# Optimization experiments

Hardware: AMD Instinct MI355X
Metric: run time of the kernel (lower is better)

## Reference

```python
import jax, jax.numpy as jnp
import numpy as np

B, C, H, W = 64, 3, 32, 32
HID, PRE, VMAX = 128, 32, 256
IN_DIM = C * 5 - 1  # 14


def setup_inputs() -> dict:
    key = jax.random.key(0)
    ks = jax.random.split(key, 9)
    s = 0.05
    return {
        "x": jax.random.uniform(ks[0], (B, C, H, W), dtype=jnp.float32),
        "W_pre": jax.random.normal(ks[1], (PRE, IN_DIM), dtype=jnp.float32) * s,
        "b_pre": jnp.zeros((PRE,), dtype=jnp.float32),
        "W_ih": jax.random.normal(ks[2], (3 * HID, PRE), dtype=jnp.float32) * s,
        "b_ih": jnp.zeros((3 * HID,), dtype=jnp.float32),
        "W_hh": jax.random.normal(ks[3], (3 * HID, HID), dtype=jnp.float32) * s,
        "b_hh": jnp.zeros((3 * HID,), dtype=jnp.float32),
        "W_post": jax.random.normal(ks[4], (VMAX, HID), dtype=jnp.float32) * s,
        "b_post": jnp.zeros((VMAX,), dtype=jnp.float32),
    }


def _img2input(x):
    # x: [b, c, h, w] -> [b, (h-2)*(w-2)*c, 5c-1], matching torch _img2input
    b, c, h, w = x.shape
    xp = jnp.transpose(x, (0, 2, 3, 1))  # [b,h,w,c]
    tl = xp[:, :-2, :-2, :]
    tc = xp[:, :-2, 1:-1, :]
    tr = xp[:, :-2, 2:, :]
    lf = xp[:, 1:-1, :-2, :]
    ct = xp[:, 1:-1, 1:-1, :]
    base = jnp.concatenate([tl, tc, tr, lf], axis=-1)  # [b,h-2,w-2,4c]
    base = jnp.broadcast_to(base[..., None, :], base.shape[:3] + (c, 4 * c))
    # tail[ic, ic1] = center[ic1] if ic1 < ic else -1
    mask = jnp.arange(c - 1)[None, :] < jnp.arange(c)[:, None]  # [c, c-1]
    tail = jnp.where(mask, ct[..., None, :c - 1], -1.0)  # [b,h-2,w-2,c,c-1]
    y = jnp.concatenate([base, tail], axis=-1)  # [b,h-2,w-2,c,5c-1]
    return y.reshape(b, (h - 2) * (w - 2) * c, 5 * c - 1)


def reference(x, W_pre, b_pre, W_ih, b_ih, W_hh, b_hh, W_post, b_post):
    b, c, h, w = x.shape
    inp = _img2input(x)                                   # [b, T, 5c-1]
    pre = jax.nn.sigmoid(inp @ W_pre.T + b_pre)           # [b, T, PRE]
    xg = pre @ W_ih.T + b_ih                              # [b, T, 3*HID]
    xg_t = jnp.transpose(xg, (1, 0, 2))                   # [T, b, 3*HID]

    def step(h_prev, xt):
        hg = h_prev @ W_hh.T + b_hh
        xr, xz, xn = jnp.split(xt, 3, axis=-1)
        hr, hz, hn = jnp.split(hg, 3, axis=-1)
        r = jax.nn.sigmoid(xr + hr)
        z = jax.nn.sigmoid(xz + hz)
        n = jnp.tanh(xn + r * hn)
        h_new = (1.0 - z) * n + z * h_prev
        return h_new, h_new

    h0 = jnp.zeros((b, W_hh.shape[1]), dtype=x.dtype)
    _, hs = jax.lax.scan(step, h0, xg_t)                  # [T, b, HID]
    hs = jnp.transpose(hs, (1, 0, 2))                     # [b, T, HID]
    out = hs @ W_post.T + b_post                          # [b, T, VMAX]
    vmax = W_post.shape[0]
    out = out.reshape(b, h - 2, w - 2, c, vmax)
    out = jnp.transpose(out, (0, 3, 1, 2, 4))             # [b, c, h-2, w-2, vmax]
    out = jnp.pad(out, ((0, 0), (0, 0), (1, 1), (1, 1), (0, 0)))
    return out  # [b, c, h, w, vmax]
```

## Files before the change

kernel.cpp:

```cpp
#include <hip/hip_runtime.h>
#include <cstdint>

#define B_    64
#define T_    2700
#define HID_  128
#define PRE_  32
#define VMAX_ 256

typedef _Float16 half2_t __attribute__((ext_vector_type(2)));
typedef _Float16 h8_t    __attribute__((ext_vector_type(8)));
union H8 { h8_t v; half2_t p[4]; };

#if __has_builtin(__builtin_amdgcn_fdot2)
__device__ __forceinline__ float FDOT2(half2_t a, half2_t b, float c) {
    return __builtin_amdgcn_fdot2(a, b, c, false);
}
#else
__device__ __forceinline__ float FDOT2(half2_t a, half2_t b, float c) {
    return c + (float)a[0] * (float)b[0] + (float)a[1] * (float)b[1];
}
#endif

__device__ __forceinline__ half2_t mk2(float a, float b) {
    half2_t r; r[0] = (_Float16)a; r[1] = (_Float16)b; return r;
}

template<int CTRL>
__device__ __forceinline__ float dpp_add(float x) {
    int t = __builtin_amdgcn_update_dpp(0, __float_as_int(x), CTRL, 0xF, 0xF, true);
    return x + __int_as_float(t);
}

__device__ __forceinline__ float fast_sigmoid(float x) {
    float t = __builtin_amdgcn_exp2f(-1.4426950408889634f * x);
    return __builtin_amdgcn_rcpf(1.0f + t);
}
__device__ __forceinline__ float fast_tanh(float x) {
    float t = __builtin_amdgcn_exp2f(2.885390081777927f * x);
    return 1.0f - 2.0f * __builtin_amdgcn_rcpf(t + 1.0f);
}
__device__ __forceinline__ void fma4(float4& a, const float4 w, const float4 h) {
    a.x += w.x * h.x; a.y += w.y * h.y; a.z += w.z * h.z; a.w += w.w * h.w;
}
__device__ __forceinline__ float hsum4(const float4 a) {
    return (a.x + a.y) + (a.z + a.w);
}

__global__ __launch_bounds__(256) void k_pre(const float* __restrict__ x,
                                             const float* __restrict__ W_pre,
                                             const float* __restrict__ b_pre,
                                             float* __restrict__ pre_out) {
    int tid  = blockIdx.x * 256 + threadIdx.x;
    int i    = tid & 31;
    int rest = tid >> 5;
    int c    = rest % 3;
    int r2   = rest / 3;
    int p    = r2 % 900;
    int b    = r2 / 900;
    int r    = p / 30;
    int cc   = p - r * 30;
    const float* xb = x + b * 3072 + r * 32 + cc;
    float f0 = xb[0],    f1  = xb[1024], f2  = xb[2048];
    float f3 = xb[1],    f4  = xb[1025], f5  = xb[2049];
    float f6 = xb[2],    f7  = xb[1026], f8  = xb[2050];
    float f9 = xb[32],   f10 = xb[1056], f11 = xb[2080];
    float ct0 = xb[33],  ct1 = xb[1057];
    float f12 = (c >= 1) ? ct0 : -1.0f;
    float f13 = (c >= 2) ? ct1 : -1.0f;
    const float* w = W_pre + i * 14;
    float d = b_pre[i];
    d += f0*w[0]  + f1*w[1]  + f2*w[2]  + f3*w[3]  + f4*w[4]  + f5*w[5]  + f6*w[6]
       + f7*w[7]  + f8*w[8]  + f9*w[9]  + f10*w[10] + f11*w[11] + f12*w[12] + f13*w[13];
    pre_out[tid] = fast_sigmoid(d);
}

__global__ __launch_bounds__(512, 1) void k_scan(const float* __restrict__ W_ih,
                                                 const float* __restrict__ b_ih,
                                                 const float* __restrict__ W_hh,
                                                 const float* __restrict__ b_hh,
                                                 const float* __restrict__ pre_in,
                                                 float* __restrict__ hs) {
    __shared__ __align__(16) _Float16 sh_h[2][HID_];
    const int tid = threadIdx.x;
    const int u   = tid >> 2;
    const int q   = tid & 3;
    const int b   = blockIdx.x;

    half2_t whr[16], whz[16], whn[16];
    {
        const float4* pr = (const float4*)(W_hh + (size_t)u * HID_ + q * 32);
        const float4* pz = (const float4*)(W_hh + (size_t)(HID_ + u) * HID_ + q * 32);
        const float4* pn = (const float4*)(W_hh + (size_t)(2 * HID_ + u) * HID_ + q * 32);
#pragma unroll
        for (int k = 0; k < 8; ++k) {
            float4 f = pr[k]; whr[2*k] = mk2(f.x, f.y); whr[2*k+1] = mk2(f.z, f.w);
        }
#pragma unroll
        for (int k = 0; k < 8; ++k) {
            float4 f = pz[k]; whz[2*k] = mk2(f.x, f.y); whz[2*k+1] = mk2(f.z, f.w);
        }
#pragma unroll
        for (int k = 0; k < 8; ++k) {
            float4 f = pn[k]; whn[2*k] = mk2(f.x, f.y); whn[2*k+1] = mk2(f.z, f.w);
        }
    }
    half2_t wir[4], wiz[4], win[4];
    {
        const float4* pr = (const float4*)(W_ih + u * PRE_ + q * 8);
        const float4* pz = (const float4*)(W_ih + (HID_ + u) * PRE_ + q * 8);
        const float4* pn = (const float4*)(W_ih + (2 * HID_ + u) * PRE_ + q * 8);
#pragma unroll
        for (int k = 0; k < 2; ++k) {
            float4 f = pr[k]; wir[2*k] = mk2(f.x, f.y); wir[2*k+1] = mk2(f.z, f.w);
            float4 g = pz[k]; wiz[2*k] = mk2(g.x, g.y); wiz[2*k+1] = mk2(g.z, g.w);
            float4 h = pn[k]; win[2*k] = mk2(h.x, h.y); win[2*k+1] = mk2(h.z, h.w);
        }
    }
    const float br  = b_ih[u] + b_hh[u];
    const float bz  = b_ih[HID_ + u] + b_hh[HID_ + u];
    const float bxn = b_ih[2 * HID_ + u];
    const float bhn = b_hh[2 * HID_ + u];

    const float* preb = pre_in + (size_t)b * T_ * PRE_ + q * 8;
    float* hsb = hs + (size_t)b * T_ * HID_;

    if (tid < HID_) { sh_h[0][tid] = (_Float16)0.f; sh_h[1][tid] = (_Float16)0.f; }
    half2_t p[4];
    {
        float4 f0 = ((const float4*)preb)[0];
        float4 f1 = ((const float4*)preb)[1];
        p[0] = mk2(f0.x, f0.y); p[1] = mk2(f0.z, f0.w);
        p[2] = mk2(f1.x, f1.y); p[3] = mk2(f1.z, f1.w);
    }
    float hu = 0.0f;
    __syncthreads();

    for (int t = 0; t < T_; ++t) {
        const int tn = (t + 1 < T_) ? (t + 1) : t;
        const float4* pnx = (const float4*)(preb + (size_t)tn * PRE_);
        float4 nf0 = pnx[0];
        float4 nf1 = pnx[1];

        const h8_t* hblk = (const h8_t*)(&sh_h[t & 1][q * 32]);
        float ar0 = FDOT2(wir[0], p[0], 0.f), ar1 = FDOT2(wir[1], p[1], 0.f);
        ar0 = FDOT2(wir[2], p[2], ar0);       ar1 = FDOT2(wir[3], p[3], ar1);
        float az0 = FDOT2(wiz[0], p[0], 0.f), az1 = FDOT2(wiz[1], p[1], 0.f);
        az0 = FDOT2(wiz[2], p[2], az0);       az1 = FDOT2(wiz[3], p[3], az1);
        float axn0 = FDOT2(win[0], p[0], 0.f), axn1 = FDOT2(win[1], p[1], 0.f);
        axn0 = FDOT2(win[2], p[2], axn0);      axn1 = FDOT2(win[3], p[3], axn1);
        float an0 = 0.f, an1 = 0.f;
#pragma unroll
        for (int k = 0; k < 4; ++k) {
            H8 hb; hb.v = hblk[k];
            ar0 = FDOT2(whr[4*k+0], hb.p[0], ar0);
            ar1 = FDOT2(whr[4*k+1], hb.p[1], ar1);
            ar0 = FDOT2(whr[4*k+2], hb.p[2], ar0);
            ar1 = FDOT2(whr[4*k+3], hb.p[3], ar1);
            az0 = FDOT2(whz[4*k+0], hb.p[0], az0);
            az1 = FDOT2(whz[4*k+1], hb.p[1], az1);
            az0 = FDOT2(whz[4*k+2], hb.p[2], az0);
            az1 = FDOT2(whz[4*k+3], hb.p[3], az1);
            an0 = FDOT2(whn[4*k+0], hb.p[0], an0);
            an1 = FDOT2(whn[4*k+1], hb.p[1], an1);
            an0 = FDOT2(whn[4*k+2], hb.p[2], an0);
            an1 = FDOT2(whn[4*k+3], hb.p[3], an1);
        }
        float sr  = ar0 + ar1;
        float sz  = az0 + az1;
        float sxn = axn0 + axn1;
        float shn = an0 + an1;
        sr  = dpp_add<0x4E>(dpp_add<0xB1>(sr));
        sz  = dpp_add<0x4E>(dpp_add<0xB1>(sz));
        sxn = dpp_add<0x4E>(dpp_add<0xB1>(sxn));
        shn = dpp_add<0x4E>(dpp_add<0xB1>(shn));

        float rg   = fast_sigmoid(sr + br);
        float zg   = fast_sigmoid(sz + bz);
        float ng   = fast_tanh(sxn + bxn + rg * (shn + bhn));
        float hnew = ng + zg * (hu - ng);
        hu = hnew;
        if (q == 0) sh_h[(t + 1) & 1][u] = (_Float16)hnew;
        __syncthreads();
        if (q == 0) hsb[(size_t)t * HID_ + u] = hnew;
        p[0] = mk2(nf0.x, nf0.y); p[1] = mk2(nf0.z, nf0.w);
        p[2] = mk2(nf1.x, nf1.y); p[3] = mk2(nf1.z, nf1.w);
    }
}

__global__ __launch_bounds__(512, 4) void k_post(const float* __restrict__ W_post,
                                                 const float* __restrict__ b_post,
                                                 const float* __restrict__ hs,
                                                 float* __restrict__ out) {
    __shared__ __align__(16) float sh[2][HID_];
    const int tid  = threadIdx.x;
    const int v    = tid >> 1;
    const int hf   = tid & 1;
    const int blk  = blockIdx.x;
    const int i    = blk & 31;
    const int rest = blk >> 5;
    const int ch   = rest % 3;
    const int b    = rest / 3;
    float* outb = out + ((size_t)(b * 3 + ch) * 1024 + i * 32) * VMAX_;

    if (i == 0 || i == 31) {
        if (hf == 0) {
#pragma unroll
            for (int jc = 0; jc < 32; ++jc) outb[jc * VMAX_ + v] = 0.0f;
        }
        return;
    }

    float4 wp[16];
    const float4* wpp = (const float4*)(W_post + (size_t)v * HID_ + hf * 64);
#pragma unroll
    for (int k = 0; k < 16; ++k) wp[k] = wpp[k];
    const float bp = b_post[v];

    const float* hsb = hs + (size_t)b * T_ * HID_;
    const int trow = (i - 1) * 30;

    if (tid < 32)
        ((float4*)sh[1])[tid] = ((const float4*)(hsb + (size_t)(trow * 3 + ch) * HID_))[tid];
    if (hf == 0) { outb[v] = 0.0f; outb[31 * VMAX_ + v] = 0.0f; }
    __syncthreads();

    for (int jc = 1; jc <= 30; ++jc) {
        if (tid < 32 && jc < 30)
            ((float4*)sh[(jc + 1) & 1])[tid] =
                ((const float4*)(hsb + (size_t)((trow + jc) * 3 + ch) * HID_))[tid];
        const float4* h4 = (const float4*)sh[jc & 1] + hf * 16;
        float4 a0 = {0,0,0,0}, a1 = {0,0,0,0}, a2 = {0,0,0,0}, a3 = {0,0,0,0};
#pragma unroll
        for (int k = 0; k < 16; k += 4) {
            fma4(a0, wp[k],     h4[k]);
            fma4(a1, wp[k + 1], h4[k + 1]);
            fma4(a2, wp[k + 2], h4[k + 2]);
            fma4(a3, wp[k + 3], h4[k + 3]);
        }
        float s = (hsum4(a0) + hsum4(a1)) + (hsum4(a2) + hsum4(a3));
        s = dpp_add<0xB1>(s);
        if (hf == 0) outb[jc * VMAX_ + v] = bp + s;
        __syncthreads();
    }
}

extern "C" void kernel_launch(void* const* d_in, const int* in_sizes, int n_in,
                              void* d_out, int out_size, void* d_ws, size_t ws_size,
                              hipStream_t stream) {
    const float* x      = (const float*)d_in[0];
    const float* W_pre  = (const float*)d_in[1];
    const float* b_pre  = (const float*)d_in[2];
    const float* W_ih   = (const float*)d_in[3];
    const float* b_ih   = (const float*)d_in[4];
    const float* W_hh   = (const float*)d_in[5];
    const float* b_hh   = (const float*)d_in[6];
    const float* W_post = (const float*)d_in[7];
    const float* b_post = (const float*)d_in[8];
    float* out = (float*)d_out;

    float* pre_buf = (float*)d_ws;
    float* hs      = pre_buf + (size_t)B_ * T_ * PRE_;

    k_pre <<<21600, 256, 0, stream>>>(x, W_pre, b_pre, pre_buf);
    k_scan<<<B_,    512, 0, stream>>>(W_ih, b_ih, W_hh, b_hh, pre_buf, hs);
    k_post<<<6144,  512, 0, stream>>>(W_post, b_post, hs, out);
}
```

Before: 2.308 ms.

## Batch four sequences per block and run GRU recurrence on MFMA

The scan kernel now processes 4 batch elements per workgroup (16 blocks instead of 64) and computes the recurrent and input projections with 16x16x16 fp16 MFMA instructions instead of per-thread fdot2 reductions. k_pre writes fp16 activations in a layout swizzled to match the MFMA B operand. Results are redistributed with ds_bpermute, and hidden-state stores are deferred by one step. Fewer, heavier blocks cut total serial latency across the batch, but only 16 CUs are used and each step carries extra permute and MFMA latency on the critical path.

```diff
diff --git a/kernel.cpp b/kernel.cpp
--- a/kernel.cpp
+++ b/kernel.cpp
@@ -6,50 +6,48 @@
 #define HID_  128
 #define PRE_  32
 #define VMAX_ 256
-
-typedef _Float16 half2_t __attribute__((ext_vector_type(2)));
-typedef _Float16 h8_t    __attribute__((ext_vector_type(8)));
-union H8 { h8_t v; half2_t p[4]; };
-
-#if __has_builtin(__builtin_amdgcn_fdot2)
-__device__ __forceinline__ float FDOT2(half2_t a, half2_t b, float c) {
-    return __builtin_amdgcn_fdot2(a, b, c, false);
-}
-#else
-__device__ __forceinline__ float FDOT2(half2_t a, half2_t b, float c) {
-    return c + (float)a[0] * (float)b[0] + (float)a[1] * (float)b[1];
-}
-#endif
-
-__device__ __forceinline__ half2_t mk2(float a, float b) {
-    half2_t r; r[0] = (_Float16)a; r[1] = (_Float16)b; return r;
-}
-
+#define NG_   16
+#define NB_   4
+
+typedef _Float16 half4_t __attribute__((ext_vector_type(4)));
+typedef float    f32x4_t __attribute__((ext_vector_type(4)));
+
+#define MFMA16(A, Bv, C) __builtin_amdgcn_mfma_f32_16x16x16f16((A), (Bv), (C), 0, 0, 0)
+
+__device__ __forceinline__ float fast_sigmoid(float x) {
+    float t = __builtin_amdgcn_exp2f(-1.4426950408889634f * x);
+    return __builtin_amdgcn_rcpf(1.0f + t);
+}
+__device__ __forceinline__ float fast_tanh(float x) {
+    float t = __builtin_amdgcn_exp2f(2.885390081777927f * x);
+    return 1.0f - 2.0f * __builtin_amdgcn_rcpf(t + 1.0f);
+}
 template<int CTRL>
 __device__ __forceinline__ float dpp_add(float x) {
     int t = __builtin_amdgcn_update_dpp(0, __float_as_int(x), CTRL, 0xF, 0xF, true);
     return x + __int_as_float(t);
 }
-
-__device__ __forceinline__ float fast_sigmoid(float x) {
-    float t = __builtin_amdgcn_exp2f(-1.4426950408889634f * x);
-    return __builtin_amdgcn_rcpf(1.0f + t);
-}
-__device__ __forceinline__ float fast_tanh(float x) {
-    float t = __builtin_amdgcn_exp2f(2.885390081777927f * x);
-    return 1.0f - 2.0f * __builtin_amdgcn_rcpf(t + 1.0f);
-}
 __device__ __forceinline__ void fma4(float4& a, const float4 w, const float4 h) {
     a.x += w.x * h.x; a.y += w.y * h.y; a.z += w.z * h.z; a.w += w.w * h.w;
 }
 __device__ __forceinline__ float hsum4(const float4 a) {
     return (a.x + a.y) + (a.z + a.w);
+}
+
+__device__ __forceinline__ float pick_reg(f32x4_t v, int addr, int sel) {
+    float t0 = __int_as_float(__builtin_amdgcn_ds_bpermute(addr, __float_as_int(v[0])));
+    float t1 = __int_as_float(__builtin_amdgcn_ds_bpermute(addr, __float_as_int(v[1])));
+    float t2 = __int_as_float(__builtin_amdgcn_ds_bpermute(addr, __float_as_int(v[2])));
+    float t3 = __int_as_float(__builtin_amdgcn_ds_bpermute(addr, __float_as_int(v[3])));
+    float a = (sel & 1) ? t1 : t0;
+    float b = (sel & 1) ? t3 : t2;
+    return (sel & 2) ? b : a;
 }
 
 __global__ __launch_bounds__(256) void k_pre(const float* __restrict__ x,
                                              const float* __restrict__ W_pre,
                                              const float* __restrict__ b_pre,
-                                             float* __restrict__ pre_out) {
+                                             _Float16* __restrict__ pre16) {
     int tid  = blockIdx.x * 256 + threadIdx.x;
     int i    = tid & 31;
     int rest = tid >> 5;
@@ -71,120 +69,128 @@
     float d = b_pre[i];
     d += f0*w[0]  + f1*w[1]  + f2*w[2]  + f3*w[3]  + f4*w[4]  + f5*w[5]  + f6*w[6]
        + f7*w[7]  + f8*w[8]  + f9*w[9]  + f10*w[10] + f11*w[11] + f12*w[12] + f13*w[13];
-    pre_out[tid] = fast_sigmoid(d);
-}
-
-__global__ __launch_bounds__(512, 1) void k_scan(const float* __restrict__ W_ih,
-                                                 const float* __restrict__ b_ih,
-                                                 const float* __restrict__ W_hh,
-                                                 const float* __restrict__ b_hh,
-                                                 const float* __restrict__ pre_in,
-                                                 float* __restrict__ hs) {
-    __shared__ __align__(16) _Float16 sh_h[2][HID_];
-    const int tid = threadIdx.x;
-    const int u   = tid >> 2;
-    const int q   = tid & 3;
-    const int b   = blockIdx.x;
-
-    half2_t whr[16], whz[16], whn[16];
-    {
-        const float4* pr = (const float4*)(W_hh + (size_t)u * HID_ + q * 32);
-        const float4* pz = (const float4*)(W_hh + (size_t)(HID_ + u) * HID_ + q * 32);
-        const float4* pn = (const float4*)(W_hh + (size_t)(2 * HID_ + u) * HID_ + q * 32);
-#pragma unroll
-        for (int k = 0; k < 8; ++k) {
-            float4 f = pr[k]; whr[2*k] = mk2(f.x, f.y); whr[2*k+1] = mk2(f.z, f.w);
-        }
-#pragma unroll
-        for (int k = 0; k < 8; ++k) {
-            float4 f = pz[k]; whz[2*k] = mk2(f.x, f.y); whz[2*k+1] = mk2(f.z, f.w);
-        }
-#pragma unroll
-        for (int k = 0; k < 8; ++k) {
-            float4 f = pn[k]; whn[2*k] = mk2(f.x, f.y); whn[2*k+1] = mk2(f.z, f.w);
-        }
-    }
-    half2_t wir[4], wiz[4], win[4];
-    {
-        const float4* pr = (const float4*)(W_ih + u * PRE_ + q * 8);
-        const float4* pz = (const float4*)(W_ih + (HID_ + u) * PRE_ + q * 8);
-        const float4* pn = (const float4*)(W_ih + (2 * HID_ + u) * PRE_ + q * 8);
-#pragma unroll
-        for (int k = 0; k < 2; ++k) {
-            float4 f = pr[k]; wir[2*k] = mk2(f.x, f.y); wir[2*k+1] = mk2(f.z, f.w);
-            float4 g = pz[k]; wiz[2*k] = mk2(g.x, g.y); wiz[2*k+1] = mk2(g.z, g.w);
-            float4 h = pn[k]; win[2*k] = mk2(h.x, h.y); win[2*k+1] = mk2(h.z, h.w);
-        }
-    }
-    const float br  = b_ih[u] + b_hh[u];
-    const float bz  = b_ih[HID_ + u] + b_hh[HID_ + u];
-    const float bxn = b_ih[2 * HID_ + u];
-    const float bhn = b_hh[2 * HID_ + u];
-
-    const float* preb = pre_in + (size_t)b * T_ * PRE_ + q * 8;
-    float* hsb = hs + (size_t)b * T_ * HID_;
-
-    if (tid < HID_) { sh_h[0][tid] = (_Float16)0.f; sh_h[1][tid] = (_Float16)0.f; }
-    half2_t p[4];
-    {
-        float4 f0 = ((const float4*)preb)[0];
-        float4 f1 = ((const float4*)preb)[1];
-        p[0] = mk2(f0.x, f0.y); p[1] = mk2(f0.z, f0.w);
-        p[2] = mk2(f1.x, f1.y); p[3] = mk2(f1.z, f1.w);
-    }
-    float hu = 0.0f;
+
+    int t  = p * 3 + c;
+    int g  = b >> 2;
+    int cs = b & 3;
+    int k  = i;
+    size_t base = ((size_t)g * T_ + t) * 128;
+    int idx = ((k >> 4) << 6) | (((k >> 2) & 3) << 4) | (cs << 2) | (k & 3);
+    pre16[base + idx] = (_Float16)fast_sigmoid(d);
+}
+
+__global__ __launch_bounds__(512) void k_scan(const float* __restrict__ W_ih,
+                                              const float* __restrict__ b_ih,
+                                              const float* __restrict__ W_hh,
+                                              const float* __restrict__ b_hh,
+                                              const _Float16* __restrict__ pre16,
+                                              float* __restrict__ hs) {
+    __shared__ __align__(16) _Float16 hbuf[2][8][4][4][4];
+
+    const int tid  = threadIdx.x;
+    const int g    = blockIdx.x;
+    const int w    = tid >> 6;
+    const int lane = tid & 63;
+    const int lo   = lane & 15;
+    const int hi   = lane >> 4;
+    const int c4   = lane & 3;
+    const int row  = w * 16 + lo;
+
+    half4_t Ar[10], Az[10], Ahn[8], Axn[2];
+#pragma unroll
+    for (int kc = 0; kc < 8; ++kc) {
+        half4_t ar, az, an;
+#pragma unroll
+        for (int j = 0; j < 4; ++j) {
+            int k = kc * 16 + hi * 4 + j;
+            ar[j] = (_Float16)W_hh[row * HID_ + k];
+            az[j] = (_Float16)W_hh[(128 + row) * HID_ + k];
+            an[j] = (_Float16)W_hh[(256 + row) * HID_ + k];
+        }
+        Ar[kc] = ar; Az[kc] = az; Ahn[kc] = an;
+    }
+#pragma unroll
+    for (int kc = 0; kc < 2; ++kc) {
+        half4_t ar, az, ax;
+#pragma unroll
+        for (int j = 0; j < 4; ++j) {
+            int k = kc * 16 + hi * 4 + j;
+            ar[j] = (_Float16)W_ih[row * PRE_ + k];
+            az[j] = (_Float16)W_ih[(128 + row) * PRE_ + k];
+            ax[j] = (_Float16)W_ih[(256 + row) * PRE_ + k];
+        }
+        Ar[8 + kc] = ar; Az[8 + kc] = az; Axn[kc] = ax;
+    }
+
+    const int u3 = w * 16 + (lane >> 2);
+    const float br  = b_ih[u3]       + b_hh[u3];
+    const float bz  = b_ih[128 + u3] + b_hh[128 + u3];
+    const float bxn = b_ih[256 + u3];
+    const float bhn = b_hh[256 + u3];
+    const int srcaddr = ((((lane >> 4) << 4) | c4) << 2);
+    const int sel     = (lane >> 2) & 3;
+
+    const char* preg = (const char*)pre16 + (size_t)g * T_ * 256;
+    float* hsb = hs + (size_t)(g * NB_ + c4) * T_ * HID_ + u3;
+
+    ((uint32_t*)hbuf)[tid] = 0u;
+
+    half4_t pf0 = *(const half4_t*)(preg + 0   + hi * 32 + c4 * 8);
+    half4_t pf1 = *(const half4_t*)(preg + 128 + hi * 32 + c4 * 8);
+    float hprev = 0.0f;
     __syncthreads();
 
     for (int t = 0; t < T_; ++t) {
+        if (t) hsb[(size_t)(t - 1) * HID_] = hprev;
         const int tn = (t + 1 < T_) ? (t + 1) : t;
-        const float4* pnx = (const float4*)(preb + (size_t)tn * PRE_);
-        float4 nf0 = pnx[0];
-        float4 nf1 = pnx[1];
-
-        const h8_t* hblk = (const h8_t*)(&sh_h[t & 1][q * 32]);
-        float ar0 = FDOT2(wir[0], p[0], 0.f), ar1 = FDOT2(wir[1], p[1], 0.f);
-        ar0 = FDOT2(wir[2], p[2], ar0);       ar1 = FDOT2(wir[3], p[3], ar1);
-        float az0 = FDOT2(wiz[0], p[0], 0.f), az1 = FDOT2(wiz[1], p[1], 0.f);
-        az0 = FDOT2(wiz[2], p[2], az0);       az1 = FDOT2(wiz[3], p[3], az1);
-        float axn0 = FDOT2(win[0], p[0], 0.f), axn1 = FDOT2(win[1], p[1], 0.f);
-        axn0 = FDOT2(win[2], p[2], axn0);      axn1 = FDOT2(win[3], p[3], axn1);
-        float an0 = 0.f, an1 = 0.f;
-#pragma unroll
-        for (int k = 0; k < 4; ++k) {
-            H8 hb; hb.v = hblk[k];
-            ar0 = FDOT2(whr[4*k+0], hb.p[0], ar0);
-            ar1 = FDOT2(whr[4*k+1], hb.p[1], ar1);
-            ar0 = FDOT2(whr[4*k+2], hb.p[2], ar0);
-            ar1 = FDOT2(whr[4*k+3], hb.p[3], ar1);
-            az0 = FDOT2(whz[4*k+0], hb.p[0], az0);
-            az1 = FDOT2(whz[4*k+1], hb.p[1], az1);
-            az0 = FDOT2(whz[4*k+2], hb.p[2], az0);
-            az1 = FDOT2(whz[4*k+3], hb.p[3], az1);
-            an0 = FDOT2(whn[4*k+0], hb.p[0], an0);
-            an1 = FDOT2(whn[4*k+1], hb.p[1], an1);
-            an0 = FDOT2(whn[4*k+2], hb.p[2], an0);
-            an1 = FDOT2(whn[4*k+3], hb.p[3], an1);
-        }
-        float sr  = ar0 + ar1;
-        float sz  = az0 + az1;
-        float sxn = axn0 + axn1;
-        float shn = an0 + an1;
-        sr  = dpp_add<0x4E>(dpp_add<0xB1>(sr));
-        sz  = dpp_add<0x4E>(dpp_add<0xB1>(sz));
-        sxn = dpp_add<0x4E>(dpp_add<0xB1>(sxn));
-        shn = dpp_add<0x4E>(dpp_add<0xB1>(shn));
-
-        float rg   = fast_sigmoid(sr + br);
-        float zg   = fast_sigmoid(sz + bz);
-        float ng   = fast_tanh(sxn + bxn + rg * (shn + bhn));
-        float hnew = ng + zg * (hu - ng);
-        hu = hnew;
-        if (q == 0) sh_h[(t + 1) & 1][u] = (_Float16)hnew;
+        half4_t pf0n = *(const half4_t*)(preg + (size_t)tn * 256 +       hi * 32 + c4 * 8);
+        half4_t pf1n = *(const half4_t*)(preg + (size_t)tn * 256 + 128 + hi * 32 + c4 * 8);
+
+        const int rb = t & 1;
+        half4_t hB[8];
+#pragma unroll
+        for (int kc = 0; kc < 8; ++kc)
+            hB[kc] = *(const half4_t*)&hbuf[rb][kc][hi][lo & 3][0];
+
+        const f32x4_t Z4 = {0.f, 0.f, 0.f, 0.f};
+        f32x4_t r0 = Z4, r1 = Z4, z0 = Z4, z1 = Z4, n0 = Z4, n1 = Z4, xs = Z4;
+#pragma unroll
+        for (int kc = 0; kc < 4; ++kc) {
+            r0 = MFMA16(Ar[kc],  hB[kc], r0);
+            z0 = MFMA16(Az[kc],  hB[kc], z0);
+            n0 = MFMA16(Ahn[kc], hB[kc], n0);
+        }
+#pragma unroll
+        for (int kc = 4; kc < 8; ++kc) {
+            r1 = MFMA16(Ar[kc],  hB[kc], r1);
+            z1 = MFMA16(Az[kc],  hB[kc], z1);
+            n1 = MFMA16(Ahn[kc], hB[kc], n1);
+        }
+        r0 = MFMA16(Ar[8], pf0, r0);  r1 = MFMA16(Ar[9], pf1, r1);
+        z0 = MFMA16(Az[8], pf0, z0);  z1 = MFMA16(Az[9], pf1, z1);
+        xs = MFMA16(Axn[0], pf0, xs); xs = MFMA16(Axn[1], pf1, xs);
+
+        f32x4_t rs = r0 + r1;
+        f32x4_t zs = z0 + z1;
+        f32x4_t ns = n0 + n1;
+
+        float srr = pick_reg(rs, srcaddr, sel) + br;
+        float szz = pick_reg(zs, srcaddr, sel) + bz;
+        float sxn = pick_reg(xs, srcaddr, sel) + bxn;
+        float shn = pick_reg(ns, srcaddr, sel) + bhn;
+
+        float rg   = fast_sigmoid(srr);
+        float zg   = fast_sigmoid(szz);
+        float ng   = fast_tanh(sxn + rg * shn);
+        float hnew = ng + zg * (hprev - ng);
+        hprev = hnew;
+
+        hbuf[rb ^ 1][w][lane >> 4][c4][(lane >> 2) & 3] = (_Float16)hnew;
+
+        pf0 = pf0n; pf1 = pf1n;
         __syncthreads();
-        if (q == 0) hsb[(size_t)t * HID_ + u] = hnew;
-        p[0] = mk2(nf0.x, nf0.y); p[1] = mk2(nf0.z, nf0.w);
-        p[2] = mk2(nf1.x, nf1.y); p[3] = mk2(nf1.z, nf1.w);
-    }
+    }
+    hsb[(size_t)(T_ - 1) * HID_] = hprev;
 }
 
 __global__ __launch_bounds__(512, 4) void k_post(const float* __restrict__ W_post,
@@ -258,10 +264,10 @@
     const float* b_post = (const float*)d_in[8];
     float* out = (float*)d_out;
 
-    float* pre_buf = (float*)d_ws;
-    float* hs      = pre_buf + (size_t)B_ * T_ * PRE_;
-
-    k_pre <<<21600, 256, 0, stream>>>(x, W_pre, b_pre, pre_buf);
-    k_scan<<<B_,    512, 0, stream>>>(W_ih, b_ih, W_hh, b_hh, pre_buf, hs);
+    _Float16* pre16 = (_Float16*)d_ws;
+    float* hs = (float*)((char*)d_ws + (size_t)NG_ * T_ * 256);
+
+    k_pre <<<21600, 256, 0, stream>>>(x, W_pre, b_pre, pre16);
+    k_scan<<<NG_,   512, 0, stream>>>(W_ih, b_ih, W_hh, b_hh, pre16, hs);
     k_post<<<6144,  512, 0, stream>>>(W_post, b_post, hs, out);
 }
```

New measurement: 2.980 ms. 29.1% more time.
